# Performance work log

Measured on AMD Instinct MI355X. Metric: run time of the kernel, lower is better.

The kernel has to match this reference:

```python
import jax, jax.numpy as jnp
import numpy as np

R_SPHERE = 1.0        # object_bounding_sphere
EPS0 = 1e-3           # initial_epsilon
N_ITERS = 30          # sphere_tracing_iters (loop body runs N_ITERS+1 times, matching torch)
SDF_TOL = 5e-7


def setup_inputs() -> dict:
    key = jax.random.key(0)
    ks = jax.random.split(key, 8)
    N, C, H = 131072, 16, 64
    return {
        "points": jax.random.normal(ks[0], (N, 3), dtype=jnp.float32),
        "cams": jax.random.normal(ks[1], (C, 3), dtype=jnp.float32),
        "W1": jax.random.normal(ks[2], (3, H), dtype=jnp.float32) * 0.5,
        "b1": jax.random.normal(ks[3], (H,), dtype=jnp.float32) * 0.1,
        "W2": jax.random.normal(ks[4], (H, H), dtype=jnp.float32) * (1.0 / np.sqrt(H)),
        "b2": jax.random.normal(ks[5], (H,), dtype=jnp.float32) * 0.1,
        "W3": jax.random.normal(ks[6], (H, 1), dtype=jnp.float32) * (1.0 / np.sqrt(H)),
        "b3": jax.random.normal(ks[7], (1,), dtype=jnp.float32) * 0.1,
    }


def reference(points, cams, W1, b1, W2, b2, W3, b3):
    # neural SDF: [..., 3] -> [...]
    def sdf(p):
        h = jax.nn.softplus(p @ W1 + b1)
        h = jax.nn.softplus(h @ W2 + b2)
        return (h @ W3 + b3)[..., 0]

    # rays from each point toward each camera: [N, C, 3]
    ray = cams[None, :, :] - points[:, None, :]
    dist_pc = jnp.linalg.norm(ray, axis=-1, keepdims=True)
    d = ray / dist_pc                                   # unit ray dirs [N, C, 3]

    # sphere intersection (far hit) for ray o + t*d, |o + t d| = r
    b = jnp.einsum("ncd,nd->nc", d, points)             # d . o
    disc = b * b - (jnp.sum(points * points, axis=-1, keepdims=True) - R_SPHERE * R_SPHERE)
    mask_intersection = disc > 0
    far = -b + jnp.sqrt(jnp.clip(disc, 0.0))            # [N, C]

    # initialization (matches torch pre-loop)
    p0 = points[:, None, :] + EPS0 * d
    cur_sdf = sdf(p0)                                   # [N, C]
    mask = cur_sdf >= 0                                 # in-progress mask
    dist = EPS0 + cur_sdf                               # distance along ray from start point

    def body(i, carry):
        cur_sdf, dist, mask = carry
        p = points[:, None, :] + dist[..., None] * d    # [N, C, 3]
        new_sdf = sdf(p)
        cur_sdf = jnp.where(mask, new_sdf, cur_sdf)     # current_sdf[mask] = new_sdf
        mask = mask & (cur_sdf >= SDF_TOL)              # mask[current_sdf < 5e-7] = 0
        dist = jnp.where(mask, dist + cur_sdf, dist)    # dist[mask] += current_sdf[mask]
        mask = mask & (dist <= far)                     # mask[dist > far] = 0
        return cur_sdf, dist, mask

    cur_sdf, dist, mask = jax.lax.fori_loop(0, N_ITERS + 1, body, (cur_sdf, dist, mask))

    visibility = (dist > far) & mask_intersection       # [N, C] bool
    return visibility
```

## Files before the change

kernel.cpp:

```cpp
#include <hip/hip_runtime.h>
#include <cmath>

#define TOTAL_RAYS (131072 * 16)
#define HDIM 64
#define NSHARD 32
#define SHARD_SZ (TOTAL_RAYS / NSHARD)
#define CHUNK 64u

typedef float v2f __attribute__((ext_vector_type(2)));
typedef float v4f __attribute__((ext_vector_type(4)));

__device__ unsigned int g_counters[NSHARD * 16];

__global__ void vis_init_counter() { g_counters[threadIdx.x * 16] = 0u; }

__device__ __forceinline__ float softplus_f(float x) {
    return fmaxf(x, 0.0f) + __logf(1.0f + __expf(-fabsf(x)));
}

extern "C" __global__ void __launch_bounds__(256, 2)
vis_trace_kernel(const float* __restrict__ points,
                 const float* __restrict__ cams,
                 const float* __restrict__ W1,
                 const float* __restrict__ b1,
                 const float* __restrict__ W2,
                 const float* __restrict__ b2,
                 const float* __restrict__ W3,
                 const float* __restrict__ b3,
                 int* __restrict__ out)
{
    const v4f* __restrict__ W2v = reinterpret_cast<const v4f*>(W2);
    const float sB3 = b3[0];

    const int lane = threadIdx.x & 63;
    int cursh = (int)((blockIdx.x * 4u + (threadIdx.x >> 6)) & (NSHARD - 1));
    int drained_cnt = 0;

    unsigned int cbase = 0u, cend = 0u;

    bool live = false, maskv = false, mint = false, drained = false;
    float ox = 0.f, oy = 0.f, oz = 0.f, dx = 0.f, dy = 0.f, dz = 0.f;
    float farv = 0.f, dist = 0.f, cur = 0.f, t = 1e-3f;
    int it = 0;
    unsigned int ridx = 0u;

    for (;;) {
        for (;;) {
            unsigned long long needm = __ballot(!live);
            if (needm == 0ull || drained) break;

            unsigned int avail = cend - cbase;
            if (avail == 0u) {
                unsigned int b = 0u;
                if (lane == 0) b = atomicAdd(&g_counters[cursh * 16], CHUNK);
                b = (unsigned int)__shfl((int)b, 0);
                if (b >= (unsigned int)SHARD_SZ) {
                    cursh = (cursh + 1) & (NSHARD - 1);
                    if (++drained_cnt >= NSHARD) drained = true;
                } else {
                    drained_cnt = 0;
                    unsigned int e = b + CHUNK;
                    if (e > (unsigned int)SHARD_SZ) e = (unsigned int)SHARD_SZ;
                    cbase = (unsigned int)cursh * SHARD_SZ + b;
                    cend  = (unsigned int)cursh * SHARD_SZ + e;
                }
                continue;
            }

            int cnt = __popcll(needm);
            unsigned int take = ((unsigned int)cnt < avail) ? (unsigned int)cnt : avail;
            unsigned int rank = (unsigned int)__popcll(needm & ((1ull << lane) - 1ull));
            if (!live && rank < take) {
                unsigned int idx = cbase + rank;
                const int n = (int)(idx >> 4), c = (int)(idx & 15u);
                const float pox = points[3 * n], poy = points[3 * n + 1], poz = points[3 * n + 2];
                const float cx = cams[3 * c], cy = cams[3 * c + 1], cz = cams[3 * c + 2];
                float tdx, tdy, tdz, tfar;
                bool tmint;
                {
                    #pragma clang fp contract(off)
                    float rx = cx - pox, ry = cy - poy, rz = cz - poz;
                    float nrm = sqrtf(rx * rx + ry * ry + rz * rz);
                    tdx = rx / nrm; tdy = ry / nrm; tdz = rz / nrm;
                    float bq = tdx * pox + tdy * poy + tdz * poz;
                    float oo = pox * pox + poy * poy + poz * poz;
                    float disc = bq * bq - (oo - 1.0f);
                    tmint = disc > 0.0f;
                    tfar = -bq + sqrtf(fmaxf(disc, 0.0f));
                }
                if (!tmint) {
                    out[idx] = 0;
                } else {
                    ridx = idx; mint = tmint; farv = tfar;
                    ox = pox; oy = poy; oz = poz;
                    dx = tdx; dy = tdy; dz = tdz;
                    live = true; maskv = true; it = 0;
                    dist = 0.f; cur = 0.f; t = 1e-3f;
                }
            }
            cbase += take;
        }
        if (__ballot(live) == 0ull) break;

        float px, py, pz;
        {
            #pragma clang fp contract(off)
            px = ox + t * dx; py = oy + t * dy; pz = oz + t * dz;
        }

        v2f acc[32];
        #pragma unroll
        for (int q = 0; q < 32; ++q) { v2f z = {0.f, 0.f}; acc[q] = z; }

        float hk;
        {
            float a0 = fmaf(pz, W1[2 * HDIM], fmaf(py, W1[HDIM], px * W1[0])) + b1[0];
            hk = softplus_f(a0);
        }

        #pragma unroll 2
        for (int k = 0; k < HDIM; ++k) {
            const int kn = (k + 1) & (HDIM - 1);
            float an = fmaf(pz, W1[2 * HDIM + kn],
                       fmaf(py, W1[HDIM + kn],
                            px * W1[kn])) + b1[kn];
            float hkn = softplus_f(an);

            v2f hk2 = {hk, hk};
            const v4f* row = &W2v[k * 16];
            #pragma unroll
            for (int q = 0; q < 16; ++q) {
                v4f w = row[q];
                v2f w0 = __builtin_shufflevector(w, w, 0, 1);
                v2f w1 = __builtin_shufflevector(w, w, 2, 3);
                acc[2 * q]     = __builtin_elementwise_fma(hk2, w0, acc[2 * q]);
                acc[2 * q + 1] = __builtin_elementwise_fma(hk2, w1, acc[2 * q + 1]);
            }
            hk = hkn;
        }

        float s3 = 0.f;
        #pragma unroll
        for (int q = 0; q < 32; ++q) {
            float h2 = softplus_f(acc[q].x + b2[2 * q]);
            s3 = fmaf(h2, W3[2 * q], s3);
            float h3 = softplus_f(acc[q].y + b2[2 * q + 1]);
            s3 = fmaf(h3, W3[2 * q + 1], s3);
        }
        const float s = s3 + sB3;

        if (live) {
            if (it == 0) {
                cur = s; maskv = (cur >= 0.0f); dist = 1e-3f + cur;
            } else {
                cur = maskv ? s : cur;
                maskv = maskv && (cur >= 5e-7f);
                dist = maskv ? (dist + cur) : dist;
                maskv = maskv && (dist <= farv);
            }
            ++it; t = dist;
            if (!maskv || it >= 32) {
                out[ridx] = ((dist > farv) && mint) ? 1 : 0;
                live = false;
            }
        }
    }
}

extern "C" void kernel_launch(void* const* d_in, const int* in_sizes, int n_in,
                              void* d_out, int out_size, void* d_ws, size_t ws_size,
                              hipStream_t stream) {
    const float* points = (const float*)d_in[0];
    const float* cams   = (const float*)d_in[1];
    const float* W1     = (const float*)d_in[2];
    const float* b1     = (const float*)d_in[3];
    const float* W2     = (const float*)d_in[4];
    const float* b2     = (const float*)d_in[5];
    const float* W3     = (const float*)d_in[6];
    const float* b3     = (const float*)d_in[7];
    int* out = (int*)d_out;

    hipLaunchKernelGGL(vis_init_counter, dim3(1), dim3(NSHARD), 0, stream);
    hipLaunchKernelGGL(vis_trace_kernel, dim3(2048), dim3(256), 0, stream,
                       points, cams, W1, b1, W2, b2, W3, b3, out);
}
```

Measured before the change: 1.104 ms.

## Cooperatively trace straggler rays across the wavefront once work queue drains

When a wavefront has drained the global work queue and has at most 16 live rays, it switches to a mode where all 64 lanes evaluate one ray's SDF together. Each lane computes one hidden unit, and the layer sums are done with cross-lane shuffles. This targets the tail, where a few long-running rays keep a mostly idle wavefront busy. The cost is serialising the remaining rays one at a time and adding many shuffles per evaluation, which could be slower if stragglers are numerous.

```diff
diff --git a/kernel.cpp b/kernel.cpp
--- a/kernel.cpp
+++ b/kernel.cpp
@@ -6,6 +6,7 @@
 #define NSHARD 32
 #define SHARD_SZ (TOTAL_RAYS / NSHARD)
 #define CHUNK 64u
+#define SOLO_MAX 16
 
 typedef float v2f __attribute__((ext_vector_type(2)));
 typedef float v4f __attribute__((ext_vector_type(4)));
@@ -100,7 +101,61 @@
             }
             cbase += take;
         }
-        if (__ballot(live) == 0ull) break;
+
+        unsigned long long lvm = __ballot(live);
+        if (lvm == 0ull) break;
+
+        if (drained && __popcll(lvm) <= SOLO_MAX) {
+            const float w1x = W1[lane], w1y = W1[HDIM + lane], w1z = W1[2 * HDIM + lane];
+            const float b1l = b1[lane], b2l = b2[lane];
+            for (;;) {
+                unsigned long long lm = __ballot(live);
+                if (lm == 0ull) break;
+                const int owner = (int)__builtin_ctzll(lm);
+                float sox = __shfl(ox, owner), soy = __shfl(oy, owner), soz = __shfl(oz, owner);
+                float sdx = __shfl(dx, owner), sdy = __shfl(dy, owner), sdz = __shfl(dz, owner);
+                float sfar = __shfl(farv, owner), sdist = __shfl(dist, owner), st = __shfl(t, owner);
+                int sit = __shfl(it, owner);
+                unsigned int srid = (unsigned int)__shfl((int)ridx, owner);
+
+                for (;;) {
+                    float px, py, pz;
+                    {
+                        #pragma clang fp contract(off)
+                        px = sox + st * sdx; py = soy + st * sdy; pz = soz + st * sdz;
+                    }
+                    float a = fmaf(pz, w1z, fmaf(py, w1y, px * w1x)) + b1l;
+                    float hk = softplus_f(a);
+                    float accj = 0.f;
+                    #pragma unroll 8
+                    for (int k = 0; k < HDIM; ++k) {
+                        float hs = __shfl(hk, k);
+                        accj = fmaf(hs, W2[k * HDIM + lane], accj);
+                    }
+                    float h2 = softplus_f(accj + b2l);
+                    float s3 = 0.f;
+                    #pragma unroll 8
+                    for (int j = 0; j < HDIM; ++j)
+                        s3 = fmaf(__shfl(h2, j), W3[j], s3);
+                    const float s = s3 + sB3;
+
+                    bool smask;
+                    if (sit == 0) {
+                        smask = (s >= 0.0f);
+                        sdist = 1e-3f + s;
+                    } else {
+                        smask = (s >= 5e-7f);
+                        sdist = smask ? (sdist + s) : sdist;
+                        smask = smask && (sdist <= sfar);
+                    }
+                    ++sit; st = sdist;
+                    if (!smask || sit >= 32) break;
+                }
+                if (lane == 0) out[srid] = (sdist > sfar) ? 1 : 0;
+                if (lane == owner) live = false;
+            }
+            break;
+        }
 
         float px, py, pz;
         {
```

Result: faster. 910.2 us (-17.5%).
